# Performance work log

Hardware: AMD Instinct MI355X
Metric: run time of the kernel (lower is better)

The kernel has to match this reference:

```python
import jax, jax.numpy as jnp
import numpy as np

# Static configuration (mirrors TemporalAugmentation with deterministic choices)
B, T_IN, N, C = 32, 512, 543, 3
SPEED = 1.2                      # fixed draw from speed_range (0.8, 1.2)
NEW_T = int(T_IN / SPEED)        # 426
JITTER_FREQ = max(1, NEW_T // 8) # 53
FRAME_DROP_P = 0.1
JITTER_STD = 0.02
NOISE_STD = 0.01
SPATIAL_STD = 0.005


def linresample(x, out_T):
    """F.interpolate(mode='linear', align_corners=True) along last axis."""
    L = x.shape[-1]
    s = jnp.arange(out_T, dtype=x.dtype) * ((L - 1) / (out_T - 1))
    i0 = jnp.clip(jnp.floor(s).astype(jnp.int32), 0, L - 2)
    frac = s - i0.astype(x.dtype)
    return x[..., i0] * (1 - frac) + x[..., i0 + 1] * frac


def setup_inputs() -> dict:
    key = jax.random.key(0)
    k1, k2, k3, k4, k5 = jax.random.split(key, 5)
    x = jax.random.normal(k1, (B, T_IN, N, C), dtype=jnp.float32)
    mask = jnp.ones((B, T_IN), dtype=bool)
    keep_mask = jax.random.bernoulli(k2, 1.0 - FRAME_DROP_P, (B, NEW_T))
    keep_mask = keep_mask.at[:, 0].set(True).at[:, -1].set(True)
    base_jitter = jax.random.normal(k3, (B, JITTER_FREQ), dtype=jnp.float32)
    noise = jax.random.normal(k4, (B, NEW_T, N, C), dtype=jnp.float32)
    spatial_noise = jax.random.normal(k5, (B, 1, N, C), dtype=jnp.float32)
    return {"x": x, "mask": mask, "keep_mask": keep_mask,
            "base_jitter": base_jitter, "noise": noise,
            "spatial_noise": spatial_noise}


def reference(x, mask, keep_mask, base_jitter, noise, spatial_noise):
    Bb, T, Nn, Cc = x.shape
    # --- speed augment: linear resample time axis T -> NEW_T ---
    xt = jnp.moveaxis(x, 1, -1)                 # (B,N,C,T)
    x = jnp.moveaxis(linresample(xt, NEW_T), -1, 1)  # (B,NEW_T,N,C)
    # nearest resample of validity mask (PyTorch 'nearest': floor(t*in/out))
    nidx = jnp.floor(jnp.arange(NEW_T) * (T / NEW_T)).astype(jnp.int32)
    mask = mask[:, nidx]
    T2 = NEW_T
    # --- frame dropout: replace dropped frames with align_corners linear
    # resample of the kept-frame subsequence (length K) back to T2 ---
    K = keep_mask.sum(axis=1)                   # (B,) kept counts
    ar = jnp.arange(T2)
    # stable order putting kept indices first, in original order
    order = jnp.argsort(jnp.where(keep_mask, ar, T2 + ar), axis=1)  # (B,T2)
    s = ar[None, :].astype(x.dtype) * (K[:, None] - 1).astype(x.dtype) / (T2 - 1)
    r0 = jnp.clip(jnp.floor(s).astype(jnp.int32), 0, (K - 2)[:, None])
    frac = (s - r0.astype(x.dtype))[:, :, None, None]
    bidx = jnp.arange(Bb)[:, None]
    idx0 = jnp.take_along_axis(order, r0, axis=1)
    idx1 = jnp.take_along_axis(order, r0 + 1, axis=1)
    interp = x[bidx, idx0] * (1 - frac) + x[bidx, idx1] * frac
    x = jnp.where(keep_mask[:, :, None, None], x, interp)
    mask = mask & keep_mask
    # --- temporal jitter: scale per-frame velocity by smooth jitter curve ---
    jit = linresample(base_jitter * JITTER_STD, T2)   # (B,T2)
    vel = x[:, 1:] - x[:, :-1]
    x = jnp.concatenate([x[:, :1], x[:, 1:] + vel * jit[:, 1:, None, None]], axis=1)
    # --- coordinate noise + per-landmark spatial noise ---
    x = x + noise * NOISE_STD + spatial_noise * SPATIAL_STD
    return x, mask
```

## Files before the change

### kernel.cpp

```cpp
#include <hip/hip_runtime.h>
#include <stdint.h>

#define B_      32
#define T_IN_   512
#define N_      543
#define C_      3
#define NEW_T_  426
#define JF_     53
#define NC_     (N_*C_)
#define XOUT_   (B_*NEW_T_*NC_)
#define NFR_    (B_*NEW_T_)
#define GPF_    408
#define FPB_    6
#define NTB_    71
#define NBLKM_  (NTB_*B_)
#define CPX_    284

#define MODE_INT   0
#define MODE_BYTE  1
#define MODE_FLOAT 2

typedef float f4u __attribute__((vector_size(16), aligned(4)));

__device__ __forceinline__ bool read_flag(const void* p, int mode, int idx) {
    if (mode == MODE_BYTE)  return ((const uint8_t*)p)[idx] != 0;
    if (mode == MODE_FLOAT) return ((const float*)p)[idx]   != 0.0f;
    return ((const int*)p)[idx] != 0;
}

__global__ __launch_bounds__(512) void prep_kernel(
    const void* __restrict__ maskp,
    const void* __restrict__ keepp,
    const float* __restrict__ bjit,
    float* __restrict__ out_mask,
    int4*  __restrict__ wsF,
    float4* __restrict__ wsW,
    float* __restrict__ wsJ)
{
    const int b = blockIdx.x;
    const int tid = threadIdx.x;

    __shared__ int flags[6];
    __shared__ int s_mode_mask, s_mode_keep;
    if (tid < 6) flags[tid] = 0;
    __syncthreads();
    if (tid < 64) {
        uint32_t vm = ((const uint32_t*)maskp)[tid];
        uint32_t vk = ((const uint32_t*)keepp)[tid];
        if (vm == 0x3F800000u)      atomicOr(&flags[2], 1);
        else if (vm > 1u)           atomicOr(&flags[1], 1);
        if (vk == 0x3F800000u)      atomicOr(&flags[5], 1);
        else if (vk > 1u)           atomicOr(&flags[4], 1);
    }
    __syncthreads();
    if (tid == 0) {
        s_mode_mask = flags[2] ? MODE_FLOAT : (flags[1] ? MODE_BYTE : MODE_INT);
        s_mode_keep = flags[5] ? MODE_FLOAT : (flags[4] ? MODE_BYTE : MODE_INT);
    }
    __syncthreads();
    const int mmode = s_mode_mask, kmode = s_mode_keep;

    __shared__ int sk[512];
    __shared__ int ps[512];
    __shared__ int kept[NEW_T_];

    int kv = 0;
    if (tid < NEW_T_) kv = read_flag(keepp, kmode, b*NEW_T_ + tid) ? 1 : 0;
    sk[tid] = (tid < NEW_T_) ? kv : 0;
    ps[tid] = sk[tid];
    __syncthreads();
    for (int off = 1; off < 512; off <<= 1) {
        int v = (tid >= off) ? ps[tid - off] : 0;
        __syncthreads();
        ps[tid] += v;
        __syncthreads();
    }
    const int K = ps[NEW_T_ - 1];
    if (tid < NEW_T_ && kv) kept[ps[tid] - 1] = tid;
    __syncthreads();

    if (tid < NEW_T_) {
        const int t = tid;
        const float RATX = (float)(511.0 / 425.0);
        float st = (float)t * RATX;
        int i0 = (int)floorf(st);
        if (i0 < 0) i0 = 0; if (i0 > T_IN_ - 2) i0 = T_IN_ - 2;
        float w = st - (float)i0;

        int4 F; float4 W;
        if (kv) {
            F = make_int4(i0, i0 + 1, i0, i0 + 1);
            W = make_float4(1.0f - w, w, 0.0f, 0.0f);
        } else {
            float s = ((float)t * (float)(K - 1)) / 425.0f;
            int r0 = (int)floorf(s);
            if (r0 < 0) r0 = 0; if (r0 > K - 2) r0 = K - 2;
            float f = s - (float)r0;
            int j0 = kept[r0], j1 = kept[r0 + 1];
            float s0 = (float)j0 * RATX;
            int a0 = (int)floorf(s0);
            if (a0 < 0) a0 = 0; if (a0 > T_IN_ - 2) a0 = T_IN_ - 2;
            float w0 = s0 - (float)a0;
            float s1 = (float)j1 * RATX;
            int a1 = (int)floorf(s1);
            if (a1 < 0) a1 = 0; if (a1 > T_IN_ - 2) a1 = T_IN_ - 2;
            float w1 = s1 - (float)a1;
            F = make_int4(a0, a0 + 1, a1, a1 + 1);
            W = make_float4((1.0f - f) * (1.0f - w0), (1.0f - f) * w0,
                            f * (1.0f - w1),          f * w1);
        }
        const int bt = b * NEW_T_ + t;
        wsF[bt] = F;
        wsW[bt] = W;

        const float RATJ = (float)(52.0 / 425.0);
        float sj = (float)t * RATJ;
        int ji = (int)floorf(sj);
        if (ji < 0) ji = 0; if (ji > JF_ - 2) ji = JF_ - 2;
        float jf = sj - (float)ji;
        float b0 = bjit[b*JF_ + ji]     * 0.02f;
        float b1 = bjit[b*JF_ + ji + 1] * 0.02f;
        float jv = b0 * (1.0f - jf) + b1 * jf;
        if (t == 0) jv = 0.0f;
        wsJ[bt] = jv;

        float mn = (float)t * (float)(512.0 / 426.0);
        int nidx = (int)floorf(mn);
        if (nidx > T_IN_ - 1) nidx = T_IN_ - 1;
        bool mo = read_flag(maskp, mmode, b*T_IN_ + nidx) && (kv != 0);
        out_mask[bt] = mo ? 1.0f : 0.0f;
    }
}

__global__ __launch_bounds__(448) __attribute__((amdgpu_waves_per_eu(4, 8)))
void main_kernel(
    const float* __restrict__ x,
    const float* __restrict__ noise,
    const float* __restrict__ spat,
    const int4*  __restrict__ wsF,
    const float4* __restrict__ wsW,
    const float* __restrict__ wsJ,
    float* __restrict__ out)
{
    const int j = threadIdx.x;
    if (j >= GPF_) return;
    const uint32_t bid = blockIdx.x;
    const uint32_t swz = (bid & 7u) * CPX_ + (bid >> 3);
    const int b  = (int)(swz / (uint32_t)NTB_);
    const int t0 = (int)(swz % (uint32_t)NTB_) * FPB_;

    uint32_t e0 = (uint32_t)j * 4u;
    if (e0 > (uint32_t)(NC_ - 4)) e0 = (uint32_t)(NC_ - 4);

    const float* __restrict__ xb = x + (size_t)b * (T_IN_ * NC_);
    const int bt0 = b * NEW_T_ + t0;

    int4   F[FPB_]; float4 W[FPB_]; float jv[FPB_];
    #pragma unroll
    for (int i = 0; i < FPB_; ++i) {
        F[i]  = wsF[bt0 + i];
        W[i]  = wsW[bt0 + i];
        jv[i] = wsJ[bt0 + i];
    }
    const int pbt = b * NEW_T_ + (t0 ? t0 - 1 : 0);
    const int4   Fp = wsF[pbt];
    const float4 Wp = wsW[pbt];

    f4u v0[FPB_], v1[FPB_], nz[FPB_];
    #pragma unroll
    for (int i = 0; i < FPB_; ++i) {
        v0[i] = *(const f4u*)(xb + (uint32_t)F[i].x * NC_ + e0);
        v1[i] = *(const f4u*)(xb + (uint32_t)F[i].y * NC_ + e0);
    }
    f4u q0 = *(const f4u*)(xb + (uint32_t)Fp.x * NC_ + e0);
    f4u q1 = *(const f4u*)(xb + (uint32_t)Fp.y * NC_ + e0);
    #pragma unroll
    for (int i = 0; i < FPB_; ++i)
        nz[i] = __builtin_nontemporal_load((const f4u*)(noise + (size_t)(bt0 + i) * NC_ + e0));
    const f4u sp = *(const f4u*)(spat + (size_t)b * NC_ + e0);

    f4u ap = Wp.x * q0 + Wp.y * q1;
    if (Wp.z != 0.0f || Wp.w != 0.0f) {
        f4u q2 = *(const f4u*)(xb + (uint32_t)Fp.z * NC_ + e0);
        f4u q3 = *(const f4u*)(xb + (uint32_t)Fp.w * NC_ + e0);
        ap += Wp.z * q2 + Wp.w * q3;
    }

    #pragma unroll
    for (int i = 0; i < FPB_; ++i) {
        f4u a = W[i].x * v0[i] + W[i].y * v1[i];
        if (W[i].z != 0.0f || W[i].w != 0.0f) {
            f4u v2 = *(const f4u*)(xb + (uint32_t)F[i].z * NC_ + e0);
            f4u v3 = *(const f4u*)(xb + (uint32_t)F[i].w * NC_ + e0);
            a += W[i].z * v2 + W[i].w * v3;
        }
        f4u r = a + (a - ap) * jv[i] + nz[i] * 0.01f + sp * 0.005f;
        *(f4u*)(out + (size_t)(bt0 + i) * NC_ + e0) = r;
        ap = a;
    }
}

extern "C" void kernel_launch(void* const* d_in, const int* in_sizes, int n_in,
                              void* d_out, int out_size, void* d_ws, size_t ws_size,
                              hipStream_t stream) {
    const float* x    = (const float*)d_in[0];
    const void*  mask = d_in[1];
    const void*  keep = d_in[2];
    const float* bjit = (const float*)d_in[3];
    const float* noise = (const float*)d_in[4];
    const float* spat  = (const float*)d_in[5];
    float* out = (float*)d_out;

    char* ws = (char*)d_ws;
    int4*   wsF = (int4*)ws;
    float4* wsW = (float4*)(ws + 218112);
    float*  wsJ = (float*)(ws + 436224);

    prep_kernel<<<B_, 512, 0, stream>>>(mask, keep, bjit,
                                        out + XOUT_, wsF, wsW, wsJ);
    main_kernel<<<NBLKM_, 448, 0, stream>>>(x, noise, spat, wsF, wsW, wsJ, out);
}
```

Baseline: 252.9 us.

## Fuse prep into main kernel and stage source rows in LDS

Merges the per-batch prep kernel into the main kernel so each block recomputes its own keep-mask prefix scan and per-frame interpolation indices and weights, which removes one launch and the workspace round trip. Each block also preloads a 9-row window of source frames into shared memory and reads interpolation inputs from LDS when they fall in that window, falling back to global loads otherwise. In exchange, every one of the 2272 blocks now redoes a 426-element scan with many barriers. The roughly 58KB of LDS per block may also limit occupancy, and the last column is handled by a separate scalar path.

```diff
diff --git a/kernel.cpp b/kernel.cpp
--- a/kernel.cpp
+++ b/kernel.cpp
@@ -9,18 +9,30 @@
 #define JF_     53
 #define NC_     (N_*C_)
 #define XOUT_   (B_*NEW_T_*NC_)
-#define NFR_    (B_*NEW_T_)
 #define GPF_    408
 #define FPB_    6
 #define NTB_    71
 #define NBLKM_  (NTB_*B_)
 #define CPX_    284
+#define WROWS_  9
+#define LROW_   1632
 
 #define MODE_INT   0
 #define MODE_BYTE  1
 #define MODE_FLOAT 2
 
 typedef float f4u __attribute__((vector_size(16), aligned(4)));
+typedef float f4a __attribute__((vector_size(16)));
+
+__device__ __forceinline__ f4u lds_ld(const float* p) {
+    f4a t = *(const f4a*)p;
+    f4u r; r[0]=t[0]; r[1]=t[1]; r[2]=t[2]; r[3]=t[3];
+    return r;
+}
+__device__ __forceinline__ void lds_st(float* p, f4u v) {
+    f4a t; t[0]=v[0]; t[1]=v[1]; t[2]=v[2]; t[3]=v[3];
+    *(f4a*)p = t;
+}
 
 __device__ __forceinline__ bool read_flag(const void* p, int mode, int idx) {
     if (mode == MODE_BYTE)  return ((const uint8_t*)p)[idx] != 0;
@@ -28,67 +40,115 @@
     return ((const int*)p)[idx] != 0;
 }
 
-__global__ __launch_bounds__(512) void prep_kernel(
-    const void* __restrict__ maskp,
-    const void* __restrict__ keepp,
+__global__ __launch_bounds__(448) __attribute__((amdgpu_waves_per_eu(3, 8)))
+void fused_kernel(
+    const float* __restrict__ x,
+    const void*  __restrict__ maskp,
+    const void*  __restrict__ keepp,
     const float* __restrict__ bjit,
-    float* __restrict__ out_mask,
-    int4*  __restrict__ wsF,
-    float4* __restrict__ wsW,
-    float* __restrict__ wsJ)
+    const float* __restrict__ noise,
+    const float* __restrict__ spat,
+    float* __restrict__ out,
+    float* __restrict__ out_mask)
 {
-    const int b = blockIdx.x;
-    const int tid = threadIdx.x;
-
-    __shared__ int flags[6];
-    __shared__ int s_mode_mask, s_mode_keep;
-    if (tid < 6) flags[tid] = 0;
-    __syncthreads();
-    if (tid < 64) {
-        uint32_t vm = ((const uint32_t*)maskp)[tid];
-        uint32_t vk = ((const uint32_t*)keepp)[tid];
+    const int j = threadIdx.x;
+    const uint32_t bid = blockIdx.x;
+    const uint32_t swz = (bid & 7u) * (uint32_t)CPX_ + (bid >> 3);
+    const int b  = (int)(swz / (uint32_t)NTB_);
+    const int t0 = (int)(swz % (uint32_t)NTB_) * FPB_;
+    const int bt0 = b * NEW_T_ + t0;
+
+    __shared__ __align__(16) float sx[WROWS_ * LROW_];
+    __shared__ int   ps[448];
+    __shared__ int   kept[NEW_T_];
+    __shared__ int   flags[6];
+    __shared__ int   s_modes[2];
+    __shared__ int4  smF[8];
+    __shared__ float4 smW[8];
+    __shared__ float smJ[8];
+
+    const float RATX = (float)(511.0 / 425.0);
+    int row_base = (int)floorf((float)t0 * RATX);
+    if (row_base < 0) row_base = 0;
+    const float* __restrict__ xb = x + (size_t)b * (T_IN_ * NC_);
+
+    uint32_t e0v = (uint32_t)j * 4u;
+    if (e0v > 1624u) e0v = 1624u;
+
+    f4u st[WROWS_]; float st_last[WROWS_];
+    #pragma unroll
+    for (int r = 0; r < WROWS_; ++r) {
+        int rr = row_base + r; if (rr > T_IN_ - 1) rr = T_IN_ - 1;
+        const float* src = xb + (size_t)rr * NC_;
+        if (j < 407)       st[r] = *(const f4u*)(src + j * 4);
+        else if (j == 407) st_last[r] = src[1628];
+    }
+    f4u nz[FPB_];
+    #pragma unroll
+    for (int i = 0; i < FPB_; ++i)
+        nz[i] = __builtin_nontemporal_load((const f4u*)(noise + (size_t)(bt0 + i) * NC_ + e0v));
+    const f4u sp = *(const f4u*)(spat + (size_t)b * NC_ + e0v);
+
+    if (j < 6) flags[j] = 0;
+    __syncthreads();
+    if (j < 64) {
+        uint32_t vm = ((const uint32_t*)maskp)[j];
+        uint32_t vk = ((const uint32_t*)keepp)[j];
         if (vm == 0x3F800000u)      atomicOr(&flags[2], 1);
         else if (vm > 1u)           atomicOr(&flags[1], 1);
         if (vk == 0x3F800000u)      atomicOr(&flags[5], 1);
         else if (vk > 1u)           atomicOr(&flags[4], 1);
     }
     __syncthreads();
-    if (tid == 0) {
-        s_mode_mask = flags[2] ? MODE_FLOAT : (flags[1] ? MODE_BYTE : MODE_INT);
-        s_mode_keep = flags[5] ? MODE_FLOAT : (flags[4] ? MODE_BYTE : MODE_INT);
-    }
-    __syncthreads();
-    const int mmode = s_mode_mask, kmode = s_mode_keep;
-
-    __shared__ int sk[512];
-    __shared__ int ps[512];
-    __shared__ int kept[NEW_T_];
+    if (j == 0) {
+        s_modes[0] = flags[2] ? MODE_FLOAT : (flags[1] ? MODE_BYTE : MODE_INT);
+        s_modes[1] = flags[5] ? MODE_FLOAT : (flags[4] ? MODE_BYTE : MODE_INT);
+    }
+    __syncthreads();
+    const int mmode = s_modes[0], kmode = s_modes[1];
+
+    const int tp = t0 ? t0 - 1 : 0;
+    const int pk = read_flag(keepp, kmode, b * NEW_T_ + tp) ? 1 : 0;
+    float stp = (float)tp * RATX;
+    int p0 = (int)floorf(stp);
+    if (p0 < 0) p0 = 0; if (p0 > T_IN_ - 2) p0 = T_IN_ - 2;
+    const float wp = stp - (float)p0;
+    f4u q0g, q1g;
+    if (pk) {
+        q0g = *(const f4u*)(xb + (uint32_t)p0 * NC_ + e0v);
+        q1g = *(const f4u*)(xb + (uint32_t)(p0 + 1) * NC_ + e0v);
+    }
 
     int kv = 0;
-    if (tid < NEW_T_) kv = read_flag(keepp, kmode, b*NEW_T_ + tid) ? 1 : 0;
-    sk[tid] = (tid < NEW_T_) ? kv : 0;
-    ps[tid] = sk[tid];
-    __syncthreads();
-    for (int off = 1; off < 512; off <<= 1) {
-        int v = (tid >= off) ? ps[tid - off] : 0;
+    if (j < NEW_T_) kv = read_flag(keepp, kmode, b * NEW_T_ + j) ? 1 : 0;
+    ps[j] = kv;
+    __syncthreads();
+    #pragma unroll
+    for (int off = 1; off < 448; off <<= 1) {
+        int v = (j >= off) ? ps[j - off] : 0;
         __syncthreads();
-        ps[tid] += v;
+        ps[j] += v;
         __syncthreads();
     }
     const int K = ps[NEW_T_ - 1];
-    if (tid < NEW_T_ && kv) kept[ps[tid] - 1] = tid;
-    __syncthreads();
-
-    if (tid < NEW_T_) {
-        const int t = tid;
-        const float RATX = (float)(511.0 / 425.0);
-        float st = (float)t * RATX;
-        int i0 = (int)floorf(st);
+    if (j < NEW_T_ && kv) kept[ps[j] - 1] = j;
+    __syncthreads();
+
+    #pragma unroll
+    for (int r = 0; r < WROWS_; ++r) {
+        if (j < 407)       lds_st(&sx[r * LROW_ + j * 4], st[r]);
+        else if (j == 407) sx[r * LROW_ + 1628] = st_last[r];
+    }
+
+    if (j < 7) {
+        const int t = (j < 6) ? (t0 + j) : tp;
+        const int kvt = read_flag(keepp, kmode, b * NEW_T_ + t) ? 1 : 0;
+        float stx = (float)t * RATX;
+        int i0 = (int)floorf(stx);
         if (i0 < 0) i0 = 0; if (i0 > T_IN_ - 2) i0 = T_IN_ - 2;
-        float w = st - (float)i0;
-
+        float w = stx - (float)i0;
         int4 F; float4 W;
-        if (kv) {
+        if (kvt) {
             F = make_int4(i0, i0 + 1, i0, i0 + 1);
             W = make_float4(1.0f - w, w, 0.0f, 0.0f);
         } else {
@@ -109,94 +169,107 @@
             W = make_float4((1.0f - f) * (1.0f - w0), (1.0f - f) * w0,
                             f * (1.0f - w1),          f * w1);
         }
-        const int bt = b * NEW_T_ + t;
-        wsF[bt] = F;
-        wsW[bt] = W;
-
-        const float RATJ = (float)(52.0 / 425.0);
-        float sj = (float)t * RATJ;
-        int ji = (int)floorf(sj);
-        if (ji < 0) ji = 0; if (ji > JF_ - 2) ji = JF_ - 2;
-        float jf = sj - (float)ji;
-        float b0 = bjit[b*JF_ + ji]     * 0.02f;
-        float b1 = bjit[b*JF_ + ji + 1] * 0.02f;
-        float jv = b0 * (1.0f - jf) + b1 * jf;
-        if (t == 0) jv = 0.0f;
-        wsJ[bt] = jv;
-
-        float mn = (float)t * (float)(512.0 / 426.0);
-        int nidx = (int)floorf(mn);
-        if (nidx > T_IN_ - 1) nidx = T_IN_ - 1;
-        bool mo = read_flag(maskp, mmode, b*T_IN_ + nidx) && (kv != 0);
-        out_mask[bt] = mo ? 1.0f : 0.0f;
-    }
-}
-
-__global__ __launch_bounds__(448) __attribute__((amdgpu_waves_per_eu(4, 8)))
-void main_kernel(
-    const float* __restrict__ x,
-    const float* __restrict__ noise,
-    const float* __restrict__ spat,
-    const int4*  __restrict__ wsF,
-    const float4* __restrict__ wsW,
-    const float* __restrict__ wsJ,
-    float* __restrict__ out)
-{
-    const int j = threadIdx.x;
-    if (j >= GPF_) return;
-    const uint32_t bid = blockIdx.x;
-    const uint32_t swz = (bid & 7u) * CPX_ + (bid >> 3);
-    const int b  = (int)(swz / (uint32_t)NTB_);
-    const int t0 = (int)(swz % (uint32_t)NTB_) * FPB_;
-
-    uint32_t e0 = (uint32_t)j * 4u;
-    if (e0 > (uint32_t)(NC_ - 4)) e0 = (uint32_t)(NC_ - 4);
-
-    const float* __restrict__ xb = x + (size_t)b * (T_IN_ * NC_);
-    const int bt0 = b * NEW_T_ + t0;
-
-    int4   F[FPB_]; float4 W[FPB_]; float jv[FPB_];
-    #pragma unroll
-    for (int i = 0; i < FPB_; ++i) {
-        F[i]  = wsF[bt0 + i];
-        W[i]  = wsW[bt0 + i];
-        jv[i] = wsJ[bt0 + i];
-    }
-    const int pbt = b * NEW_T_ + (t0 ? t0 - 1 : 0);
-    const int4   Fp = wsF[pbt];
-    const float4 Wp = wsW[pbt];
-
-    f4u v0[FPB_], v1[FPB_], nz[FPB_];
-    #pragma unroll
-    for (int i = 0; i < FPB_; ++i) {
-        v0[i] = *(const f4u*)(xb + (uint32_t)F[i].x * NC_ + e0);
-        v1[i] = *(const f4u*)(xb + (uint32_t)F[i].y * NC_ + e0);
-    }
-    f4u q0 = *(const f4u*)(xb + (uint32_t)Fp.x * NC_ + e0);
-    f4u q1 = *(const f4u*)(xb + (uint32_t)Fp.y * NC_ + e0);
-    #pragma unroll
-    for (int i = 0; i < FPB_; ++i)
-        nz[i] = __builtin_nontemporal_load((const f4u*)(noise + (size_t)(bt0 + i) * NC_ + e0));
-    const f4u sp = *(const f4u*)(spat + (size_t)b * NC_ + e0);
-
-    f4u ap = Wp.x * q0 + Wp.y * q1;
-    if (Wp.z != 0.0f || Wp.w != 0.0f) {
-        f4u q2 = *(const f4u*)(xb + (uint32_t)Fp.z * NC_ + e0);
-        f4u q3 = *(const f4u*)(xb + (uint32_t)Fp.w * NC_ + e0);
-        ap += Wp.z * q2 + Wp.w * q3;
-    }
-
-    #pragma unroll
-    for (int i = 0; i < FPB_; ++i) {
-        f4u a = W[i].x * v0[i] + W[i].y * v1[i];
-        if (W[i].z != 0.0f || W[i].w != 0.0f) {
-            f4u v2 = *(const f4u*)(xb + (uint32_t)F[i].z * NC_ + e0);
-            f4u v3 = *(const f4u*)(xb + (uint32_t)F[i].w * NC_ + e0);
-            a += W[i].z * v2 + W[i].w * v3;
-        }
-        f4u r = a + (a - ap) * jv[i] + nz[i] * 0.01f + sp * 0.005f;
-        *(f4u*)(out + (size_t)(bt0 + i) * NC_ + e0) = r;
-        ap = a;
+        smF[j] = F; smW[j] = W;
+        if (j < 6) {
+            const float RATJ = (float)(52.0 / 425.0);
+            float sj = (float)t * RATJ;
+            int ji = (int)floorf(sj);
+            if (ji < 0) ji = 0; if (ji > JF_ - 2) ji = JF_ - 2;
+            float jf = sj - (float)ji;
+            float b0 = bjit[b * JF_ + ji]     * 0.02f;
+            float b1 = bjit[b * JF_ + ji + 1] * 0.02f;
+            float jv2 = b0 * (1.0f - jf) + b1 * jf;
+            if (t == 0) jv2 = 0.0f;
+            smJ[j] = jv2;
+            float mn = (float)t * (float)(512.0 / 426.0);
+            int nidx = (int)floorf(mn);
+            if (nidx > T_IN_ - 1) nidx = T_IN_ - 1;
+            bool mo = read_flag(maskp, mmode, b * T_IN_ + nidx) && (kvt != 0);
+            out_mask[b * NEW_T_ + t] = mo ? 1.0f : 0.0f;
+        }
+    }
+    __syncthreads();
+
+    if (j < GPF_) {
+        f4u ap;
+        if (pk) {
+            ap = (1.0f - wp) * q0g + wp * q1g;
+        } else {
+            const int4 Fp = smF[6]; const float4 Wp = smW[6];
+            f4u q0 = *(const f4u*)(xb + (uint32_t)Fp.x * NC_ + e0v);
+            f4u q1 = *(const f4u*)(xb + (uint32_t)Fp.y * NC_ + e0v);
+            ap = Wp.x * q0 + Wp.y * q1;
+            if (Wp.z != 0.0f || Wp.w != 0.0f) {
+                f4u q2 = *(const f4u*)(xb + (uint32_t)Fp.z * NC_ + e0v);
+                f4u q3 = *(const f4u*)(xb + (uint32_t)Fp.w * NC_ + e0v);
+                ap += Wp.z * q2 + Wp.w * q3;
+            }
+        }
+        #pragma unroll
+        for (int i = 0; i < FPB_; ++i) {
+            const int4 F = smF[i]; const float4 W = smW[i]; const float jvi = smJ[i];
+            const int rlx = F.x - row_base;
+            f4u v0, v1;
+            if ((unsigned)rlx < (unsigned)(WROWS_ - 1)) {
+                v0 = lds_ld(&sx[rlx * LROW_ + e0v]);
+                v1 = lds_ld(&sx[(rlx + 1) * LROW_ + e0v]);
+            } else {
+                v0 = *(const f4u*)(xb + (uint32_t)F.x * NC_ + e0v);
+                v1 = *(const f4u*)(xb + (uint32_t)F.y * NC_ + e0v);
+            }
+            f4u a = W.x * v0 + W.y * v1;
+            if (W.z != 0.0f || W.w != 0.0f) {
+                const int rlz = F.z - row_base;
+                f4u v2, v3;
+                if ((unsigned)rlz < (unsigned)(WROWS_ - 1)) {
+                    v2 = lds_ld(&sx[rlz * LROW_ + e0v]);
+                    v3 = lds_ld(&sx[(rlz + 1) * LROW_ + e0v]);
+                } else {
+                    v2 = *(const f4u*)(xb + (uint32_t)F.z * NC_ + e0v);
+                    v3 = *(const f4u*)(xb + (uint32_t)F.w * NC_ + e0v);
+                }
+                a += W.z * v2 + W.w * v3;
+            }
+            f4u r = a + (a - ap) * jvi + nz[i] * 0.01f + sp * 0.005f;
+            *(f4u*)(out + (size_t)(bt0 + i) * NC_ + e0v) = r;
+            ap = a;
+        }
+
+        if (j == 407) {
+            const int4 Fp2 = smF[6]; const float4 Wp2 = smW[6];
+            float aps = Wp2.x * xb[(uint32_t)Fp2.x * NC_ + 1628]
+                      + Wp2.y * xb[(uint32_t)Fp2.y * NC_ + 1628];
+            if (Wp2.z != 0.0f || Wp2.w != 0.0f)
+                aps += Wp2.z * xb[(uint32_t)Fp2.z * NC_ + 1628]
+                     + Wp2.w * xb[(uint32_t)Fp2.w * NC_ + 1628];
+            const float sps = spat[(size_t)b * NC_ + 1628];
+            #pragma unroll
+            for (int i = 0; i < FPB_; ++i) {
+                const int4 F = smF[i]; const float4 W = smW[i];
+                const int rlx = F.x - row_base;
+                float v0s, v1s;
+                if ((unsigned)rlx < (unsigned)(WROWS_ - 1)) {
+                    v0s = sx[rlx * LROW_ + 1628]; v1s = sx[(rlx + 1) * LROW_ + 1628];
+                } else {
+                    v0s = xb[(uint32_t)F.x * NC_ + 1628]; v1s = xb[(uint32_t)F.y * NC_ + 1628];
+                }
+                float as = W.x * v0s + W.y * v1s;
+                if (W.z != 0.0f || W.w != 0.0f) {
+                    const int rlz = F.z - row_base;
+                    float v2s, v3s;
+                    if ((unsigned)rlz < (unsigned)(WROWS_ - 1)) {
+                        v2s = sx[rlz * LROW_ + 1628]; v3s = sx[(rlz + 1) * LROW_ + 1628];
+                    } else {
+                        v2s = xb[(uint32_t)F.z * NC_ + 1628]; v3s = xb[(uint32_t)F.w * NC_ + 1628];
+                    }
+                    as += W.z * v2s + W.w * v3s;
+                }
+                float nzs = noise[(size_t)(bt0 + i) * NC_ + 1628];
+                float rs = as + (as - aps) * smJ[i] + nzs * 0.01f + sps * 0.005f;
+                out[(size_t)(bt0 + i) * NC_ + 1628] = rs;
+                aps = as;
+            }
+        }
     }
 }
 
@@ -211,12 +284,6 @@
     const float* spat  = (const float*)d_in[5];
     float* out = (float*)d_out;
 
-    char* ws = (char*)d_ws;
-    int4*   wsF = (int4*)ws;
-    float4* wsW = (float4*)(ws + 218112);
-    float*  wsJ = (float*)(ws + 436224);
-
-    prep_kernel<<<B_, 512, 0, stream>>>(mask, keep, bjit,
-                                        out + XOUT_, wsF, wsW, wsJ);
-    main_kernel<<<NBLKM_, 448, 0, stream>>>(x, noise, spat, wsF, wsW, wsJ, out);
-}
+    fused_kernel<<<NBLKM_, 448, 0, stream>>>(x, mask, keep, bjit, noise, spat,
+                                             out, out + XOUT_);
+}
```

Result: slower. 269.1 us (+6.4%).
